# Kernel tuning notes

Measured on AMD Instinct MI355X. Metric: run time of the kernel, lower is better.

The kernel has to match this reference:

```python
import jax, jax.numpy as jnp
import numpy as np

B, N, D = 32, 1024, 512
NUM_CLASSES = 4
LN_EPS = 1e-5


def _layer_norm(x, g, b):
    mu = jnp.mean(x, axis=-1, keepdims=True)
    var = jnp.mean(jnp.square(x - mu), axis=-1, keepdims=True)
    return (x - mu) * jax.lax.rsqrt(var + LN_EPS) * g + b


def setup_inputs() -> dict:
    key = jax.random.key(0)
    ks = jax.random.split(key, 8)
    s = 0.05
    inp = {
        "sc_matrix": jax.random.uniform(ks[0], (B, N, N), dtype=jnp.float32),
        # GCN encoder params
        "W1": jax.random.normal(ks[1], (N, D), dtype=jnp.float32) * s,
        "b1": jnp.zeros((D,), jnp.float32),
        "W2": jax.random.normal(ks[2], (D, D), dtype=jnp.float32) * s,
        "b2": jnp.zeros((D,), jnp.float32),
        "ln_g": jnp.ones((D,), jnp.float32),
        "ln_b": jnp.zeros((D,), jnp.float32),
        # classifier params
        "Wc1": jax.random.normal(ks[3], (D, 128), dtype=jnp.float32) * s,
        "bc1": jnp.zeros((128,), jnp.float32),
        "g1": jnp.ones((128,), jnp.float32),
        "t1": jnp.zeros((128,), jnp.float32),
        "Wc2": jax.random.normal(ks[4], (128, 64), dtype=jnp.float32) * s,
        "bc2": jnp.zeros((64,), jnp.float32),
        "g2": jnp.ones((64,), jnp.float32),
        "t2": jnp.zeros((64,), jnp.float32),
        "Wc3": jax.random.normal(ks[5], (64, NUM_CLASSES), dtype=jnp.float32) * s,
        "bc3": jnp.zeros((NUM_CLASSES,), jnp.float32),
    }
    return inp


def reference(sc_matrix, W1, b1, W2, b2, ln_g, ln_b,
              Wc1, bc1, g1, t1, Wc2, bc2, g2, t2, Wc3, bc3):
    # Every entry of sc_matrix is nonzero, so the edge list covers all (i,j)
    # pairs incl. self-loops; GCN message passing == dense normalized matmul.
    # PyG gcn_norm: deg[j] = sum_i A[i,j]; out = D^-1/2 A^T D^-1/2 h.
    A = sc_matrix                              # [B,N,N], A[b,i,j] = edge i->j
    deg = jnp.sum(A, axis=-2)                  # col sums, [B,N]
    dis = jnp.where(deg > 0, jax.lax.rsqrt(deg), 0.0)   # deg^{-1/2}
    An = jnp.swapaxes(A, -1, -2) * dis[:, :, None] * dis[:, None, :]  # [B,N,N]

    x = sc_matrix                              # node features = SC rows [B,N,N]
    h = jax.nn.relu(jnp.matmul(An, jnp.matmul(x, W1)) + b1)   # conv1+relu [B,N,D]
    h = jnp.matmul(An, jnp.matmul(h, W2)) + b2                # conv2      [B,N,D]
    z = _layer_norm(h, ln_g, ln_b)

    z_pooled = jnp.mean(z, axis=1)             # [B,D]

    c = jax.nn.relu(_layer_norm(z_pooled @ Wc1 + bc1, g1, t1))
    c = jax.nn.relu(_layer_norm(c @ Wc2 + bc2, g2, t2))
    logits = c @ Wc3 + bc3                     # [B,num_classes]
    return (logits, z_pooled)
```

## Files before the change

kernel.cpp:

```cpp
#include <hip/hip_runtime.h>
#include <hip/hip_bf16.h>

#define B_ 32
#define N_ 1024
#define D_ 512
#define LN_EPS 1e-5f

using bf16 = __bf16;
using bf16x4 = __attribute__((ext_vector_type(4))) __bf16;
using bf16x8 = __attribute__((ext_vector_type(8))) __bf16;
using floatx4 = __attribute__((ext_vector_type(4))) float;

__device__ __forceinline__ void gld16(const bf16* gp, bf16* lp) {
  __builtin_amdgcn_global_load_lds(
      (const __attribute__((address_space(1))) void*)gp,
      (__attribute__((address_space(3))) void*)lp, 16, 0, 0);
}

__global__ __launch_bounds__(256) void k_deg(const float* __restrict__ A,
                                             float* __restrict__ deg,
                                             bf16* __restrict__ Abf) {
  int b = blockIdx.y;
  int i0 = blockIdx.x * 32;
  int t = threadIdx.x;
  const float* p = A + (size_t)b * N_ * N_ + (size_t)i0 * N_ + t * 4;
  bf16* op = Abf + (size_t)b * N_ * N_ + (size_t)i0 * N_ + t * 4;
  float4 acc = {0.f, 0.f, 0.f, 0.f};
  #pragma unroll 4
  for (int i = 0; i < 32; ++i) {
    float4 v = *(const float4*)(p + (size_t)i * N_);
    acc.x += v.x; acc.y += v.y; acc.z += v.z; acc.w += v.w;
    bf16x4 o = {(bf16)v.x, (bf16)v.y, (bf16)v.z, (bf16)v.w};
    *(bf16x4*)(op + (size_t)i * N_) = o;
  }
  float* d = deg + b * N_ + t * 4;
  atomicAdd(d + 0, acc.x); atomicAdd(d + 1, acc.y);
  atomicAdd(d + 2, acc.z); atomicAdd(d + 3, acc.w);
}

__global__ __launch_bounds__(256) void k_rsqrt(float* __restrict__ d) {
  int i = blockIdx.x * 256 + threadIdx.x;
  float v = d[i];
  d[i] = v > 0.f ? rsqrtf(v) : 0.f;
}

__global__ __launch_bounds__(256) void k_build(const bf16* __restrict__ Abf,
                                               const float* __restrict__ dis,
                                               bf16* __restrict__ Anbf) {
  __shared__ float tile[64][65];
  int b = blockIdx.z;
  int i0 = blockIdx.x * 64;
  int j0 = blockIdx.y * 64;
  int t = threadIdx.x;
  const bf16* Ab = Abf + (size_t)b * N_ * N_;
  bf16* Anb = Anbf + (size_t)b * N_ * N_;
  #pragma unroll
  for (int cc = 0; cc < 4; ++cc) {
    int chunk = cc * 256 + t;
    int r = chunk >> 4;
    int c4 = (chunk & 15) << 2;
    bf16x4 v = *(const bf16x4*)(Ab + (size_t)(j0 + r) * N_ + i0 + c4);
    tile[r][c4 + 0] = (float)v[0]; tile[r][c4 + 1] = (float)v[1];
    tile[r][c4 + 2] = (float)v[2]; tile[r][c4 + 3] = (float)v[3];
  }
  __syncthreads();
  const float* disb = dis + b * N_;
  #pragma unroll
  for (int cc = 0; cc < 4; ++cc) {
    int chunk = cc * 256 + t;
    int ii = chunk >> 4;
    int jj4 = (chunk & 15) << 2;
    float di = disb[i0 + ii];
    bf16x4 o;
    #pragma unroll
    for (int e = 0; e < 4; ++e)
      o[e] = (bf16)(tile[jj4 + e][ii] * di * disb[j0 + jj4 + e]);
    *(bf16x4*)(Anb + (size_t)(i0 + ii) * N_ + j0 + jj4) = o;
  }
}

__global__ __launch_bounds__(256) void k_transpose(const float* __restrict__ in,
                                                   bf16* __restrict__ out,
                                                   int R, int C) {
  __shared__ float tile[64][65];
  int c0 = blockIdx.x * 64;
  int r0 = blockIdx.y * 64;
  int t = threadIdx.x;
  #pragma unroll
  for (int cc = 0; cc < 4; ++cc) {
    int idx = cc * 256 + t;
    int r = idx >> 4, c4 = (idx & 15) << 2;
    const float4 v = *(const float4*)(in + (size_t)(r0 + r) * C + c0 + c4);
    tile[r][c4 + 0] = v.x; tile[r][c4 + 1] = v.y;
    tile[r][c4 + 2] = v.z; tile[r][c4 + 3] = v.w;
  }
  __syncthreads();
  #pragma unroll
  for (int cc = 0; cc < 4; ++cc) {
    int idx = cc * 256 + t;
    int c = idx >> 4, r4 = (idx & 15) << 2;
    bf16* dst = out + (size_t)(c0 + c) * R + r0 + r4;
    #pragma unroll
    for (int e = 0; e < 4; ++e) dst[e] = (bf16)tile[r4 + e][c];
  }
}

template <bool BIAS, bool RELU>
__global__ __launch_bounds__(256) void k_gemm(
    const bf16* __restrict__ Abase, size_t strideA,
    const bf16* __restrict__ Btbase, size_t strideBt,
    bf16* __restrict__ Cbase, size_t strideC,
    const float* __restrict__ bias, int Nn, int K) {
  __shared__ bf16 sA[128 * 64];
  __shared__ bf16 sB[128 * 64];
  int nxy = gridDim.x * gridDim.y;
  int L = blockIdx.z * nxy + blockIdx.y * gridDim.x + blockIdx.x;
  int b = (L & 7) + 8 * (L / (nxy * 8));
  int inner = (L >> 3) % nxy;
  int n0 = (inner % gridDim.x) * 128;
  int m0 = (inner / gridDim.x) * 128;

  const bf16* A = Abase + (size_t)b * strideA;
  const bf16* Bt = Btbase + (size_t)b * strideBt;
  int t = threadIdx.x;
  int lane = t & 63, wid = t >> 6;
  int wm = (wid >> 1) * 64, wn = (wid & 1) * 64;
  int l16 = lane & 15, q = lane >> 4;

  int rowoff = lane >> 3;
  int schunk = (lane & 7) ^ rowoff;
  const bf16* agp = A + (size_t)(m0 + wid * 32 + rowoff) * K + schunk * 8;
  const bf16* bgp = Bt + (size_t)(n0 + wid * 32 + rowoff) * K + schunk * 8;
  bf16* alp = &sA[wid * 2048 + lane * 8];
  bf16* blp = &sB[wid * 2048 + lane * 8];

  int xorb = l16 & 7;
  int co[2] = {(q ^ xorb) * 8, ((q + 4) ^ xorb) * 8};

  floatx4 acc[4][4];
  #pragma unroll
  for (int i = 0; i < 4; ++i)
    #pragma unroll
    for (int j = 0; j < 4; ++j) acc[i][j] = (floatx4){0.f, 0.f, 0.f, 0.f};

  for (int kt = 0; kt < K; kt += 64) {
    #pragma unroll
    for (int s = 0; s < 4; ++s) {
      gld16(agp + (size_t)s * 8 * K + kt, alp + s * 512);
      gld16(bgp + (size_t)s * 8 * K + kt, blp + s * 512);
    }
    __syncthreads();
    #pragma unroll
    for (int h = 0; h < 2; ++h) {
      bf16x8 af[4], bfr[4];
      #pragma unroll
      for (int mt = 0; mt < 4; ++mt)
        af[mt] = *(const bf16x8*)(&sA[(wm + mt * 16 + l16) * 64 + co[h]]);
      #pragma unroll
      for (int nt = 0; nt < 4; ++nt)
        bfr[nt] = *(const bf16x8*)(&sB[(wn + nt * 16 + l16) * 64 + co[h]]);
      #pragma unroll
      for (int mt = 0; mt < 4; ++mt)
        #pragma unroll
        for (int nt = 0; nt < 4; ++nt)
          acc[mt][nt] = __builtin_amdgcn_mfma_f32_16x16x32_bf16(
              af[mt], bfr[nt], acc[mt][nt], 0, 0, 0);
    }
    __syncthreads();
  }

  bf16* C = Cbase + (size_t)b * strideC;
  #pragma unroll
  for (int mt = 0; mt < 4; ++mt)
    #pragma unroll
    for (int nt = 0; nt < 4; ++nt)
      #pragma unroll
      for (int r = 0; r < 4; ++r) {
        int row = m0 + wm + mt * 16 + q * 4 + r;
        int col = n0 + wn + nt * 16 + l16;
        float v = acc[mt][nt][r];
        if (BIAS) v += bias[col];
        if (RELU) v = v > 0.f ? v : 0.f;
        C[(size_t)row * Nn + col] = (bf16)v;
      }
}

__global__ __launch_bounds__(256) void k_lnpool(const bf16* __restrict__ H2,
                                                const float* __restrict__ g,
                                                const float* __restrict__ be,
                                                float* __restrict__ zp_accum) {
  int b = blockIdx.y;
  int r0 = blockIdx.x * 64;
  int t = threadIdx.x, lane = t & 63, w = t >> 6;
  float ge[8], bee[8];
  #pragma unroll
  for (int e = 0; e < 8; ++e) { ge[e] = g[lane * 8 + e]; bee[e] = be[lane * 8 + e]; }
  float acc[8] = {0, 0, 0, 0, 0, 0, 0, 0};
  for (int rr = 0; rr < 16; ++rr) {
    int row = r0 + w * 16 + rr;
    const bf16* p = H2 + ((size_t)b * N_ + row) * D_ + lane * 8;
    bf16x8 hv = *(const bf16x8*)p;
    float x[8];
    float s = 0.f;
    #pragma unroll
    for (int e = 0; e < 8; ++e) { x[e] = (float)hv[e]; s += x[e]; }
    #pragma unroll
    for (int off = 32; off; off >>= 1) s += __shfl_xor(s, off);
    float mu = s * (1.f / 512.f);
    float ss = 0.f;
    #pragma unroll
    for (int e = 0; e < 8; ++e) { float d = x[e] - mu; ss += d * d; }
    #pragma unroll
    for (int off = 32; off; off >>= 1) ss += __shfl_xor(ss, off);
    float rs = rsqrtf(ss * (1.f / 512.f) + LN_EPS);
    #pragma unroll
    for (int e = 0; e < 8; ++e) acc[e] += (x[e] - mu) * rs * ge[e] + bee[e];
  }
  __shared__ float part[4][512];
  #pragma unroll
  for (int e = 0; e < 8; ++e) part[w][lane * 8 + e] = acc[e];
  __syncthreads();
  #pragma unroll
  for (int k = 0; k < 2; ++k) {
    int d = t + k * 256;
    float s4 = part[0][d] + part[1][d] + part[2][d] + part[3][d];
    atomicAdd(&zp_accum[b * D_ + d], s4);
  }
}

__global__ __launch_bounds__(128) void k_cls(
    const float* __restrict__ zp_accum,
    const float* __restrict__ Wc1, const float* __restrict__ bc1,
    const float* __restrict__ g1, const float* __restrict__ t1,
    const float* __restrict__ Wc2, const float* __restrict__ bc2,
    const float* __restrict__ g2, const float* __restrict__ t2,
    const float* __restrict__ Wc3, const float* __restrict__ bc3,
    float* __restrict__ out) {
  __shared__ float z[512];
  __shared__ float c1s[128];
  __shared__ float c2s[64];
  __shared__ float red[128];
  int b = blockIdx.x, t = threadIdx.x;
  #pragma unroll
  for (int k = 0; k < 4; ++k) {
    int d = t + k * 128;
    float v = zp_accum[b * 512 + d] * (1.f / 1024.f);
    z[d] = v;
    out[128 + b * 512 + d] = v;
  }
  __syncthreads();
  float y = bc1[t];
  for (int d = 0; d < 512; ++d) y += z[d] * Wc1[d * 128 + t];
  red[t] = y;
  __syncthreads();
  float mu = 0.f;
  for (int k = 0; k < 128; ++k) mu += red[k];
  mu *= (1.f / 128.f);
  float var = 0.f;
  for (int k = 0; k < 128; ++k) { float dd = red[k] - mu; var += dd * dd; }
  var *= (1.f / 128.f);
  float c = (y - mu) * rsqrtf(var + LN_EPS) * g1[t] + t1[t];
  c1s[t] = c > 0.f ? c : 0.f;
  __syncthreads();
  if (t < 64) {
    float y2 = bc2[t];
    for (int k = 0; k < 128; ++k) y2 += c1s[k] * Wc2[k * 64 + t];
    red[t] = y2;
  }
  __syncthreads();
  if (t < 64) {
    float mu2 = 0.f;
    for (int k = 0; k < 64; ++k) mu2 += red[k];
    mu2 *= (1.f / 64.f);
    float v2 = 0.f;
    for (int k = 0; k < 64; ++k) { float dd = red[k] - mu2; v2 += dd * dd; }
    v2 *= (1.f / 64.f);
    float cc = (red[t] - mu2) * rsqrtf(v2 + LN_EPS) * g2[t] + t2[t];
    c2s[t] = cc > 0.f ? cc : 0.f;
  }
  __syncthreads();
  if (t < 4) {
    float y3 = bc3[t];
    for (int k = 0; k < 64; ++k) y3 += c2s[k] * Wc3[k * 4 + t];
    out[b * 4 + t] = y3;
  }
}

extern "C" void kernel_launch(void* const* d_in, const int* in_sizes, int n_in,
                              void* d_out, int out_size, void* d_ws, size_t ws_size,
                              hipStream_t stream) {
  const float* A   = (const float*)d_in[0];
  const float* W1  = (const float*)d_in[1];
  const float* b1  = (const float*)d_in[2];
  const float* W2  = (const float*)d_in[3];
  const float* b2  = (const float*)d_in[4];
  const float* lng = (const float*)d_in[5];
  const float* lnb = (const float*)d_in[6];
  const float* Wc1 = (const float*)d_in[7];
  const float* bc1 = (const float*)d_in[8];
  const float* g1  = (const float*)d_in[9];
  const float* t1  = (const float*)d_in[10];
  const float* Wc2 = (const float*)d_in[11];
  const float* bc2 = (const float*)d_in[12];
  const float* g2  = (const float*)d_in[13];
  const float* t2  = (const float*)d_in[14];
  const float* Wc3 = (const float*)d_in[15];
  const float* bc3 = (const float*)d_in[16];
  float* out = (float*)d_out;

  char* ws = (char*)d_ws;
  size_t off = 0;
  auto alloc = [&](size_t bytes) {
    char* p = ws + off;
    off += (bytes + 255) & ~(size_t)255;
    return p;
  };
  float* dis  = (float*)alloc((size_t)B_ * N_ * 4);
  bf16* Anbf  = (bf16*)alloc((size_t)B_ * N_ * N_ * 2);
  bf16* W1t   = (bf16*)alloc((size_t)D_ * N_ * 2);
  bf16* W2t   = (bf16*)alloc((size_t)D_ * D_ * 2);
  bf16* T12t  = (bf16*)alloc((size_t)B_ * D_ * N_ * 2);
  bf16* H1    = (bf16*)alloc((size_t)B_ * N_ * D_ * 2);
  bf16* Abf   = (bf16*)alloc((size_t)B_ * N_ * N_ * 2);
  bf16* H2    = Abf;
  float* zp   = (float*)alloc((size_t)B_ * D_ * 4);

  hipMemsetAsync(dis, 0, (size_t)B_ * N_ * 4, stream);
  hipMemsetAsync(zp, 0, (size_t)B_ * D_ * 4, stream);

  k_deg<<<dim3(32, B_), 256, 0, stream>>>(A, dis, Abf);
  k_rsqrt<<<B_ * N_ / 256, 256, 0, stream>>>(dis);
  k_build<<<dim3(16, 16, B_), 256, 0, stream>>>(Abf, dis, Anbf);
  k_transpose<<<dim3(8, 16), 256, 0, stream>>>(W1, W1t, N_, D_);
  k_transpose<<<dim3(8, 8), 256, 0, stream>>>(W2, W2t, D_, D_);

  k_gemm<false, false><<<dim3(8, 4, B_), 256, 0, stream>>>(
      W1t, 0, Abf, (size_t)N_ * N_, T12t, (size_t)D_ * N_, nullptr, N_, N_);
  k_gemm<true, true><<<dim3(4, 8, B_), 256, 0, stream>>>(
      Anbf, (size_t)N_ * N_, T12t, (size_t)D_ * N_, H1, (size_t)N_ * D_, b1, D_, N_);
  k_gemm<false, false><<<dim3(8, 4, B_), 256, 0, stream>>>(
      W2t, 0, H1, (size_t)N_ * D_, T12t, (size_t)D_ * N_, nullptr, N_, D_);
  k_gemm<true, false><<<dim3(4, 8, B_), 256, 0, stream>>>(
      Anbf, (size_t)N_ * N_, T12t, (size_t)D_ * N_, H2, (size_t)N_ * D_, b2, D_, N_);

  k_lnpool<<<dim3(16, B_), 256, 0, stream>>>(H2, lng, lnb, zp);
  k_cls<<<B_, 128, 0, stream>>>(zp, Wc1, bc1, g1, t1, Wc2, bc2, g2, t2, Wc3, bc3, out);
}
```

Before: 459.5 us.

## Fuse rsqrt into build, merge weight transposes, enlarge deg blocks, add occupancy hint

Removes the separate rsqrt kernel by computing inverse square-root degrees in shared memory inside the normalized-adjacency build kernel. The two weight transposes are merged into one launch. The degree kernel now processes 128 rows per block, so there are fewer atomics and blocks. The GEMM gets a min-blocks-per-CU launch bound and computes the swizzle offset inline. The intent is fewer launches and less overhead, at the cost of fewer blocks in k_deg (256 total) and possible register pressure in the GEMM.

```diff
diff --git a/kernel.cpp b/kernel.cpp
--- a/kernel.cpp
+++ b/kernel.cpp
@@ -21,13 +21,13 @@
                                              float* __restrict__ deg,
                                              bf16* __restrict__ Abf) {
   int b = blockIdx.y;
-  int i0 = blockIdx.x * 32;
+  int i0 = blockIdx.x * 128;
   int t = threadIdx.x;
   const float* p = A + (size_t)b * N_ * N_ + (size_t)i0 * N_ + t * 4;
   bf16* op = Abf + (size_t)b * N_ * N_ + (size_t)i0 * N_ + t * 4;
   float4 acc = {0.f, 0.f, 0.f, 0.f};
   #pragma unroll 4
-  for (int i = 0; i < 32; ++i) {
+  for (int i = 0; i < 128; ++i) {
     float4 v = *(const float4*)(p + (size_t)i * N_);
     acc.x += v.x; acc.y += v.y; acc.z += v.z; acc.w += v.w;
     bf16x4 o = {(bf16)v.x, (bf16)v.y, (bf16)v.z, (bf16)v.w};
@@ -38,22 +38,24 @@
   atomicAdd(d + 2, acc.z); atomicAdd(d + 3, acc.w);
 }
 
-__global__ __launch_bounds__(256) void k_rsqrt(float* __restrict__ d) {
-  int i = blockIdx.x * 256 + threadIdx.x;
-  float v = d[i];
-  d[i] = v > 0.f ? rsqrtf(v) : 0.f;
-}
-
 __global__ __launch_bounds__(256) void k_build(const bf16* __restrict__ Abf,
-                                               const float* __restrict__ dis,
+                                               const float* __restrict__ deg,
                                                bf16* __restrict__ Anbf) {
   __shared__ float tile[64][65];
+  __shared__ float disI[64], disJ[64];
   int b = blockIdx.z;
   int i0 = blockIdx.x * 64;
   int j0 = blockIdx.y * 64;
   int t = threadIdx.x;
   const bf16* Ab = Abf + (size_t)b * N_ * N_;
   bf16* Anb = Anbf + (size_t)b * N_ * N_;
+  if (t < 64) {
+    float v = deg[b * N_ + i0 + t];
+    disI[t] = v > 0.f ? rsqrtf(v) : 0.f;
+  } else if (t < 128) {
+    float v = deg[b * N_ + j0 + (t - 64)];
+    disJ[t - 64] = v > 0.f ? rsqrtf(v) : 0.f;
+  }
   #pragma unroll
   for (int cc = 0; cc < 4; ++cc) {
     int chunk = cc * 256 + t;
@@ -64,27 +66,35 @@
     tile[r][c4 + 2] = (float)v[2]; tile[r][c4 + 3] = (float)v[3];
   }
   __syncthreads();
-  const float* disb = dis + b * N_;
   #pragma unroll
   for (int cc = 0; cc < 4; ++cc) {
     int chunk = cc * 256 + t;
     int ii = chunk >> 4;
     int jj4 = (chunk & 15) << 2;
-    float di = disb[i0 + ii];
+    float di = disI[ii];
     bf16x4 o;
     #pragma unroll
     for (int e = 0; e < 4; ++e)
-      o[e] = (bf16)(tile[jj4 + e][ii] * di * disb[j0 + jj4 + e]);
+      o[e] = (bf16)(tile[jj4 + e][ii] * di * disJ[jj4 + e]);
     *(bf16x4*)(Anb + (size_t)(i0 + ii) * N_ + j0 + jj4) = o;
   }
 }
 
-__global__ __launch_bounds__(256) void k_transpose(const float* __restrict__ in,
-                                                   bf16* __restrict__ out,
-                                                   int R, int C) {
+__global__ __launch_bounds__(256) void k_transpose(const float* __restrict__ W1,
+                                                   bf16* __restrict__ W1t,
+                                                   const float* __restrict__ W2,
+                                                   bf16* __restrict__ W2t) {
   __shared__ float tile[64][65];
-  int c0 = blockIdx.x * 64;
-  int r0 = blockIdx.y * 64;
+  int blk = blockIdx.x;
+  const float* in; bf16* outp; int R, C, c0, r0;
+  if (blk < 128) {
+    in = W1; outp = W1t; R = N_; C = D_;
+    c0 = (blk & 7) * 64; r0 = (blk >> 3) * 64;
+  } else {
+    blk -= 128;
+    in = W2; outp = W2t; R = D_; C = D_;
+    c0 = (blk & 7) * 64; r0 = (blk >> 3) * 64;
+  }
   int t = threadIdx.x;
   #pragma unroll
   for (int cc = 0; cc < 4; ++cc) {
@@ -99,14 +109,14 @@
   for (int cc = 0; cc < 4; ++cc) {
     int idx = cc * 256 + t;
     int c = idx >> 4, r4 = (idx & 15) << 2;
-    bf16* dst = out + (size_t)(c0 + c) * R + r0 + r4;
+    bf16* dst = outp + (size_t)(c0 + c) * R + r0 + r4;
     #pragma unroll
     for (int e = 0; e < 4; ++e) dst[e] = (bf16)tile[r4 + e][c];
   }
 }
 
 template <bool BIAS, bool RELU>
-__global__ __launch_bounds__(256) void k_gemm(
+__global__ __launch_bounds__(256, 4) void k_gemm(
     const bf16* __restrict__ Abase, size_t strideA,
     const bf16* __restrict__ Btbase, size_t strideBt,
     bf16* __restrict__ Cbase, size_t strideC,
@@ -135,7 +145,6 @@
   bf16* blp = &sB[wid * 2048 + lane * 8];
 
   int xorb = l16 & 7;
-  int co[2] = {(q ^ xorb) * 8, ((q + 4) ^ xorb) * 8};
 
   floatx4 acc[4][4];
   #pragma unroll
@@ -152,13 +161,14 @@
     __syncthreads();
     #pragma unroll
     for (int h = 0; h < 2; ++h) {
+      int cko = ((q + 4 * h) ^ xorb) * 8;
       bf16x8 af[4], bfr[4];
       #pragma unroll
       for (int mt = 0; mt < 4; ++mt)
-        af[mt] = *(const bf16x8*)(&sA[(wm + mt * 16 + l16) * 64 + co[h]]);
+        af[mt] = *(const bf16x8*)(&sA[(wm + mt * 16 + l16) * 64 + cko]);
       #pragma unroll
       for (int nt = 0; nt < 4; ++nt)
-        bfr[nt] = *(const bf16x8*)(&sB[(wn + nt * 16 + l16) * 64 + co[h]]);
+        bfr[nt] = *(const bf16x8*)(&sB[(wn + nt * 16 + l16) * 64 + cko]);
       #pragma unroll
       for (int mt = 0; mt < 4; ++mt)
         #pragma unroll
@@ -315,7 +325,7 @@
     off += (bytes + 255) & ~(size_t)255;
     return p;
   };
-  float* dis  = (float*)alloc((size_t)B_ * N_ * 4);
+  float* deg  = (float*)alloc((size_t)B_ * N_ * 4);
   bf16* Anbf  = (bf16*)alloc((size_t)B_ * N_ * N_ * 2);
   bf16* W1t   = (bf16*)alloc((size_t)D_ * N_ * 2);
   bf16* W2t   = (bf16*)alloc((size_t)D_ * D_ * 2);
@@ -325,14 +335,12 @@
   bf16* H2    = Abf;
   float* zp   = (float*)alloc((size_t)B_ * D_ * 4);
 
-  hipMemsetAsync(dis, 0, (size_t)B_ * N_ * 4, stream);
+  hipMemsetAsync(deg, 0, (size_t)B_ * N_ * 4, stream);
   hipMemsetAsync(zp, 0, (size_t)B_ * D_ * 4, stream);
 
-  k_deg<<<dim3(32, B_), 256, 0, stream>>>(A, dis, Abf);
-  k_rsqrt<<<B_ * N_ / 256, 256, 0, stream>>>(dis);
-  k_build<<<dim3(16, 16, B_), 256, 0, stream>>>(Abf, dis, Anbf);
-  k_transpose<<<dim3(8, 16), 256, 0, stream>>>(W1, W1t, N_, D_);
-  k_transpose<<<dim3(8, 8), 256, 0, stream>>>(W2, W2t, D_, D_);
+  k_deg<<<dim3(8, B_), 256, 0, stream>>>(A, deg, Abf);
+  k_build<<<dim3(16, 16, B_), 256, 0, stream>>>(Abf, deg, Anbf);
+  k_transpose<<<192, 256, 0, stream>>>(W1, W1t, W2, W2t);
 
   k_gemm<false, false><<<dim3(8, 4, B_), 256, 0, stream>>>(
       W1t, 0, Abf, (size_t)N_ * N_, T12t, (size_t)D_ * N_, nullptr, N_, N_);
```

Result: faster. 430.9 us (-6.2%).
